# Kernel tuning notes

Measured on AMD Instinct MI355X. Metric: run time of the kernel, lower is better.

The kernel has to match this reference:

```python
import jax, jax.numpy as jnp
import numpy as np

B, N, D, H, NDIMS, NS = 4, 1024, 512, 8, 3, 1
HD = D // H


def setup_inputs() -> dict:
    key = jax.random.key(0)
    ks = jax.random.split(key, 10)
    x = jax.random.normal(ks[0], (B, N, D), dtype=jnp.float32)
    coords = jax.random.normal(ks[1], (B, N, NDIMS), dtype=jnp.float32)
    # pad last 64 key positions in half the batch
    key_padding_mask = jnp.zeros((B, N), dtype=bool).at[: B // 2, -64:].set(True)
    s = 1.0 / np.sqrt(D)
    Wqkv = jax.random.normal(ks[2], (3 * D, D), dtype=jnp.float32) * s  # torch Linear weight [out,in]
    Wout = jax.random.normal(ks[3], (D, D), dtype=jnp.float32) * s
    bout = jnp.zeros((D,), dtype=jnp.float32)
    fin = NDIMS + 1  # num_dims>1 -> dist channel appended
    W1 = jax.random.normal(ks[4], (H * 4, fin), dtype=jnp.float32) / np.sqrt(fin)
    b1 = jnp.zeros((H * 4,), dtype=jnp.float32)
    W2 = jax.random.normal(ks[5], (H, H * 4), dtype=jnp.float32) / np.sqrt(H * 4)
    b2 = jnp.zeros((H,), dtype=jnp.float32)
    bias_alpha = jax.random.normal(ks[6], (1,), dtype=jnp.float32)
    return dict(x=x, coords=coords, key_padding_mask=key_padding_mask,
                bias_alpha=bias_alpha, W1=W1, b1=b1, W2=W2, b2=b2,
                Wqkv=Wqkv, Wout=Wout, bout=bout)


def reference(x, coords, key_padding_mask, bias_alpha, W1, b1, W2, b2, Wqkv, Wout, bout):
    scale = HD ** (-0.5)
    qkv = x @ Wqkv.T  # [B,N,3D]
    q, k, v = jnp.split(qkv, 3, axis=-1)
    q = q.reshape(B, N, H, HD).transpose(0, 2, 1, 3)  # [B,H,N,HD]
    k = k.reshape(B, N, H, HD).transpose(0, 2, 1, 3)
    v = v.reshape(B, N, H, HD).transpose(0, 2, 1, 3)

    dpos = coords[:, :, None, :] - coords[:, None, :, :]  # [B,N,N,ndims]
    dist = jnp.linalg.norm(dpos, axis=-1, keepdims=True)
    dpos = jnp.concatenate([dpos, dist], axis=-1)  # [B,N,N,ndims+1]
    h = jax.nn.gelu(dpos @ W1.T + b1, approximate=False)
    bias = (h @ W2.T + b2).transpose(0, 3, 1, 2)  # [B,H,N,N]
    # zero bias rows/cols for special tokens
    valid = jnp.arange(N) >= NS
    bias = bias * (valid[:, None] & valid[None, :])[None, None]

    dots = jnp.einsum('bhid,bhjd->bhij', q, k) * scale
    logits = dots + bias_alpha[0] * bias
    logits = jnp.where(key_padding_mask[:, None, None, :], -jnp.inf, logits)
    attn = jax.nn.softmax(logits, axis=-1)
    out = jnp.einsum('bhij,bhjd->bhid', attn, v)
    out = out.transpose(0, 2, 1, 3).reshape(B, N, D)
    return out @ Wout.T + bout, attn
```

## Files before the change

### kernel.cpp

```cpp
#include <hip/hip_runtime.h>
#include <hip/hip_fp16.h>
#include <stdint.h>
#include <math.h>

#define B_  4
#define N_  1024
#define D_  512
#define H_  8
#define HD_ 64

typedef short s16x8 __attribute__((ext_vector_type(8)));
typedef float f32x4 __attribute__((ext_vector_type(4)));

__device__ __forceinline__ unsigned short f2bf(float f) {
    unsigned u = __float_as_uint(f);
    u += 0x7fffu + ((u >> 16) & 1u);
    return (unsigned short)(u >> 16);
}
__device__ __forceinline__ float bf2f(unsigned short h) {
    return __uint_as_float(((unsigned)h) << 16);
}

__device__ __forceinline__ float fast_gelu(float x) {
    float ax = fabsf(x) * 0.7071067811865476f;
    float t  = __builtin_amdgcn_rcpf(fmaf(0.3275911f, ax, 1.0f));
    float e  = __expf(-ax * ax);
    float poly = t * fmaf(t, fmaf(t, fmaf(t, fmaf(t, 1.061405429f, -1.453152027f),
                                          1.421413741f), -0.284496736f), 0.254829592f);
    float erfv = 1.0f - poly * e;
    float s = copysignf(erfv, x);
    return 0.5f * x * (1.0f + s);
}

__global__ void k_split(const float* __restrict__ s, unsigned short* __restrict__ h,
                        unsigned short* __restrict__ l, int n) {
    int i = blockIdx.x * 256 + threadIdx.x;
    if (i < n) {
        float x = s[i];
        unsigned short hb = f2bf(x);
        h[i] = hb;
        l[i] = f2bf(x - bf2f(hb));
    }
}

__global__ void k_mask_detect(const unsigned char* __restrict__ m, int* __restrict__ flag) {
    __shared__ int s;
    if (threadIdx.x == 0) s = 0;
    __syncthreads();
    int found = 0;
    for (int i = threadIdx.x; i < B_ * N_; i += 256)
        if ((i & 3) && m[i]) found = 1;
    if (found) atomicOr(&s, 1);
    __syncthreads();
    if (threadIdx.x == 0) flag[0] = s;
}

__global__ __launch_bounds__(256) void k_gemm3(
    const unsigned short* __restrict__ Ah, const unsigned short* __restrict__ Al,
    const unsigned short* __restrict__ Bwh, const unsigned short* __restrict__ Bwl,
    float* __restrict__ C, const float* __restrict__ bias, int M, int Nn, int K)
{
    constexpr int BM = 64, BN = 128, BK = 64;
    __shared__ unsigned short At[BM * BK];
    __shared__ unsigned short Bt[BN * BK];
    const int tid = threadIdx.x, lane = tid & 63, wid = tid >> 6;
    const int m0 = blockIdx.x * BM, n0 = blockIdx.y * BN;
    const int wm = wid >> 1, wn = wid & 1;
    f32x4 acc[2][4] = {};
    const unsigned short* Aps[3] = {Ah, Ah, Al};
    const unsigned short* Bps[3] = {Bwh, Bwl, Bwh};

    for (int combo = 0; combo < 3; ++combo) {
        const unsigned short* __restrict__ Ap = Aps[combo];
        const unsigned short* __restrict__ Bp = Bps[combo];
        for (int k0 = 0; k0 < K; k0 += BK) {
            s16x8 sa[2], sb[4];
            #pragma unroll
            for (int r = 0; r < 2; ++r) {
                int s = r * 256 + tid, row = s >> 3, c8 = s & 7;
                sa[r] = *(const s16x8*)(Ap + (size_t)(m0 + row) * K + k0 + c8 * 8);
            }
            #pragma unroll
            for (int r = 0; r < 4; ++r) {
                int s = r * 256 + tid, row = s >> 3, c8 = s & 7;
                sb[r] = *(const s16x8*)(Bp + (size_t)(n0 + row) * K + k0 + c8 * 8);
            }
            __syncthreads();
            #pragma unroll
            for (int r = 0; r < 2; ++r) { int s = r * 256 + tid; *(s16x8*)(At + s * 8) = sa[r]; }
            #pragma unroll
            for (int r = 0; r < 4; ++r) { int s = r * 256 + tid; *(s16x8*)(Bt + s * 8) = sb[r]; }
            __syncthreads();
            #pragma unroll
            for (int kk = 0; kk < BK; kk += 32) {
                s16x8 a[2], bb[4];
                #pragma unroll
                for (int fm = 0; fm < 2; ++fm)
                    a[fm] = *(const s16x8*)(At + (wm * 32 + fm * 16 + (lane & 15)) * BK + kk + (lane >> 4) * 8);
                #pragma unroll
                for (int fn = 0; fn < 4; ++fn)
                    bb[fn] = *(const s16x8*)(Bt + (wn * 64 + fn * 16 + (lane & 15)) * BK + kk + (lane >> 4) * 8);
                #pragma unroll
                for (int fm = 0; fm < 2; ++fm)
                    #pragma unroll
                    for (int fn = 0; fn < 4; ++fn)
                        acc[fm][fn] = __builtin_amdgcn_mfma_f32_16x16x32_bf16(a[fm], bb[fn], acc[fm][fn], 0, 0, 0);
            }
        }
    }
    #pragma unroll
    for (int fm = 0; fm < 2; ++fm)
        #pragma unroll
        for (int fn = 0; fn < 4; ++fn)
            #pragma unroll
            for (int r = 0; r < 4; ++r) {
                int row  = m0 + wm * 32 + fm * 16 + (lane >> 4) * 4 + r;
                int coln = n0 + wn * 64 + fn * 16 + (lane & 15);
                float v = acc[fm][fn][r];
                if (bias) v += bias[coln];
                C[(size_t)row * Nn + coln] = v;
            }
}

__global__ void k_rearrange(const float* __restrict__ qkv, unsigned short* __restrict__ qp,
                            unsigned short* __restrict__ kp) {
    int t = blockIdx.x * 256 + threadIdx.x;
    int d = t & 63, n = (t >> 6) & 1023, h = (t >> 16) & 7, b = t >> 19;
    const float* src = qkv + ((size_t)(b * N_ + n)) * (3 * D_) + h * HD_ + d;
    float q = src[0], k = src[D_];
    unsigned short qh = f2bf(q), ql = f2bf(q - bf2f(qh));
    unsigned short kh = f2bf(k), kl = f2bf(k - bf2f(kh));
    size_t base = ((size_t)(b * H_ + h) * N_ + n) * 128;
    qp[base + d] = qh; qp[base + 64 + d] = ql;
    kp[base + d] = kh; kp[base + 64 + d] = kl;
}

__global__ void k_vtrans(const float* __restrict__ qkv, unsigned short* __restrict__ vT) {
    __shared__ unsigned short T[64][65];
    int n0 = blockIdx.x * 64, h = blockIdx.y, b = blockIdx.z;
    int tid = threadIdx.x;
    #pragma unroll
    for (int rep = 0; rep < 16; ++rep) {
        int idx = rep * 256 + tid;
        int nl = idx >> 6, d = idx & 63;
        T[nl][d] = f2bf(qkv[((size_t)(b * N_ + n0 + nl)) * (3 * D_) + 2 * D_ + h * HD_ + d]);
    }
    __syncthreads();
    #pragma unroll
    for (int rep = 0; rep < 16; ++rep) {
        int idx = rep * 256 + tid;
        int dl = idx >> 6, nl = idx & 63;
        vT[((size_t)(b * H_ + h) * HD_ + dl) * N_ + n0 + nl] = T[nl][dl];
    }
}

__global__ __launch_bounds__(256) void k_bias(
    const float* __restrict__ coords, const float* __restrict__ alpha,
    const float* __restrict__ W1, const float* __restrict__ b1,
    const float* __restrict__ W2, const float* __restrict__ b2,
    unsigned short* __restrict__ biasH)
{
    __shared__ float sW1[128], sb1[32], sW2[256], sb2[8];
    int tid = threadIdx.x;
    if (tid < 128) sW1[tid] = W1[tid];
    if (tid < 32)  sb1[tid] = b1[tid];
    sW2[tid] = W2[tid];
    if (tid < 8)   sb2[tid] = b2[tid];
    __syncthreads();

    size_t t = (size_t)blockIdx.x * 256 + tid;
    int j = (int)(t & 1023), i = (int)((t >> 10) & 1023), b = (int)(t >> 20);
    const float* ci = coords + ((size_t)b * N_ + i) * 3;
    const float* cj = coords + ((size_t)b * N_ + j) * 3;
    float dx = ci[0] - cj[0], dy = ci[1] - cj[1], dz = ci[2] - cj[2];
    float dist = sqrtf(dx * dx + dy * dy + dz * dz);

    float acc[8];
    #pragma unroll
    for (int hh = 0; hh < 8; ++hh) acc[hh] = sb2[hh];

    #pragma unroll 1
    for (int g = 0; g < 4; ++g) {
        float gg[8];
        #pragma unroll
        for (int cc = 0; cc < 8; ++cc) {
            int c = g * 8 + cc;
            float p = fmaf(sW1[c * 4], dx,
                      fmaf(sW1[c * 4 + 1], dy,
                      fmaf(sW1[c * 4 + 2], dz,
                      fmaf(sW1[c * 4 + 3], dist, sb1[c]))));
            gg[cc] = fast_gelu(p);
        }
        #pragma unroll
        for (int hh = 0; hh < 8; ++hh)
            #pragma unroll
            for (int cc = 0; cc < 8; ++cc)
                acc[hh] = fmaf(sW2[hh * 32 + g * 8 + cc], gg[cc], acc[hh]);
    }

    float vfac = (i >= 1 && j >= 1) ? alpha[0] : 0.f;
    #pragma unroll
    for (int hh = 0; hh < 8; ++hh) {
        __half hv = __float2half(vfac * acc[hh]);
        biasH[(((size_t)(b * H_ + hh)) * N_ + i) * N_ + j] = *(unsigned short*)&hv;
    }
}

__global__ __launch_bounds__(256, 3) void k_attn(
    const unsigned short* __restrict__ qp, const unsigned short* __restrict__ kp,
    const unsigned short* __restrict__ vT,
    const unsigned short* __restrict__ biasH,
    float* __restrict__ attnout,
    const unsigned char* __restrict__ mraw, const int* __restrict__ flag,
    unsigned short* __restrict__ avh, unsigned short* __restrict__ avl)
{
    __shared__ s16x8 pool16[2048];
    __shared__ unsigned char smask[N_];
    __shared__ float redm[16][4];
    __shared__ float reds[16][4];
    const int tid = threadIdx.x, lane = tid & 63, wid = tid >> 6;

    int flat = blockIdx.x + 64 * (blockIdx.y + 8 * blockIdx.z);
    int swz  = (flat & 7) * 256 + (flat >> 3);
    const int i0 = (swz & 63) * 16;
    const int h  = (swz >> 6) & 7;
    const int b  = swz >> 9;
    const size_t bh = (size_t)(b * H_ + h);
    const int g = lane >> 4;
    const int cl = lane & 15;

    if (flag[0] != 0) {
        for (int i2 = tid; i2 < N_; i2 += 256) smask[i2] = mraw[b * N_ + i2];
    } else {
        const int* mi = (const int*)mraw;
        for (int i2 = tid; i2 < N_; i2 += 256) smask[i2] = (unsigned char)(mi[b * N_ + i2] != 0);
    }

    const unsigned short* qrow = qp + (bh * N_ + i0 + cl) * 128 + g * 8;
    s16x8 aqh0 = *(const s16x8*)(qrow);
    s16x8 aqh1 = *(const s16x8*)(qrow + 32);
    s16x8 aql0 = *(const s16x8*)(qrow + 64);
    s16x8 aql1 = *(const s16x8*)(qrow + 96);

    int soff[4];
    #pragma unroll
    for (int p = 0; p < 4; ++p) {
        int o = p * 4096 + tid * 16;
        int row = o >> 8, offl = o & 255;
        soff[p] = row * 128 + ((offl ^ ((row & 7) << 4)) >> 1);
    }
    const unsigned short* kbase = kp + bh * (size_t)N_ * 128;

    const int lr = wid * 16 + cl;
    int rdoff[4];
    #pragma unroll
    for (int f = 0; f < 4; ++f)
        rdoff[f] = lr * 256 + ((g * 16 + f * 64) ^ ((lr & 7) << 4));

    char* poolb = (char*)pool16;

    {
        s16x8 st[4];
        #pragma unroll
        for (int p = 0; p < 4; ++p) st[p] = *(const s16x8*)(kbase + soff[p]);
        #pragma unroll
        for (int p = 0; p < 4; ++p) *(s16x8*)(poolb + p * 4096 + tid * 16) = st[p];
    }
    __syncthreads();

    f32x4 acc[16];
    #pragma unroll
    for (int c = 0; c < 16; ++c) {
        s16x8 st[4];
        if (c < 15) {
            const unsigned short* cb = kbase + (size_t)(c + 1) * 8192;
            #pragma unroll
            for (int p = 0; p < 4; ++p) st[p] = *(const s16x8*)(cb + soff[p]);
        }
        char* kb = poolb + (c & 1) * 16384;
        s16x8 k0 = *(const s16x8*)(kb + rdoff[0]);
        s16x8 k1 = *(const s16x8*)(kb + rdoff[1]);
        s16x8 k2 = *(const s16x8*)(kb + rdoff[2]);
        s16x8 k3 = *(const s16x8*)(kb + rdoff[3]);
        f32x4 a = {0.f, 0.f, 0.f, 0.f};
        a = __builtin_amdgcn_mfma_f32_16x16x32_bf16(aqh0, k0, a, 0, 0, 0);
        a = __builtin_amdgcn_mfma_f32_16x16x32_bf16(aqh1, k1, a, 0, 0, 0);
        a = __builtin_amdgcn_mfma_f32_16x16x32_bf16(aqh0, k2, a, 0, 0, 0);
        a = __builtin_amdgcn_mfma_f32_16x16x32_bf16(aqh1, k3, a, 0, 0, 0);
        a = __builtin_amdgcn_mfma_f32_16x16x32_bf16(aql0, k0, a, 0, 0, 0);
        a = __builtin_amdgcn_mfma_f32_16x16x32_bf16(aql1, k1, a, 0, 0, 0);
        acc[c] = a;
        if (c < 15) {
            char* wb = poolb + ((c + 1) & 1) * 16384;
            #pragma unroll
            for (int p = 0; p < 4; ++p) *(s16x8*)(wb + p * 4096 + tid * 16) = st[p];
        }
        __syncthreads();
    }

    {
        unsigned short* bl = (unsigned short*)poolb;
        const unsigned short* bsrc = biasH + (bh * N_ + i0) * N_;
        #pragma unroll
        for (int p2 = 0; p2 < 8; ++p2) {
            int idx = p2 * 256 + tid;
            *(s16x8*)(bl + idx * 8) = *(const s16x8*)(bsrc + (size_t)idx * 8);
        }
    }
    __syncthreads();

    const float scale = 0.125f;
    const unsigned short* bl = (const unsigned short*)poolb;
    #pragma unroll
    for (int j = 0; j < 16; ++j) {
        const int col = (j * 4 + wid) * 16 + cl;
        const bool mj = (smask[col] != 0);
        #pragma unroll
        for (int r = 0; r < 4; ++r) {
            unsigned short u = bl[(g * 4 + r) * 1024 + col];
            float bv = __half2float(*(const __half*)&u);
            acc[j][r] = mj ? -1e30f : fmaf(acc[j][r], scale, bv);
        }
    }

    float m[4];
    #pragma unroll
    for (int r = 0; r < 4; ++r) {
        float mm = acc[0][r];
        #pragma unroll
        for (int j = 1; j < 16; ++j) mm = fmaxf(mm, acc[j][r]);
        m[r] = mm;
    }
    #pragma unroll
    for (int msk = 1; msk < 16; msk <<= 1)
        #pragma unroll
        for (int r = 0; r < 4; ++r) m[r] = fmaxf(m[r], __shfl_xor(m[r], msk));
    if (cl == 0)
        #pragma unroll
        for (int r = 0; r < 4; ++r) redm[g * 4 + r][wid] = m[r];
    __syncthreads();
    #pragma unroll
    for (int r = 0; r < 4; ++r) {
        int row = g * 4 + r;
        m[r] = fmaxf(fmaxf(redm[row][0], redm[row][1]), fmaxf(redm[row][2], redm[row][3]));
    }

    float s[4] = {0.f, 0.f, 0.f, 0.f};
    #pragma unroll
    for (int j = 0; j < 16; ++j)
        #pragma unroll
        for (int r = 0; r < 4; ++r) {
            float e = __expf(acc[j][r] - m[r]);
            acc[j][r] = e;
            s[r] += e;
        }
    #pragma unroll
    for (int msk = 1; msk < 16; msk <<= 1)
        #pragma unroll
        for (int r = 0; r < 4; ++r) s[r] += __shfl_xor(s[r], msk);
    if (cl == 0)
        #pragma unroll
        for (int r = 0; r < 4; ++r) reds[g * 4 + r][wid] = s[r];
    __syncthreads();
    float sinv[4];
    #pragma unroll
    for (int r = 0; r < 4; ++r) {
        int row = g * 4 + r;
        sinv[r] = 1.0f / (reds[row][0] + reds[row][1] + reds[row][2] + reds[row][3]);
    }

    float* gattn = attnout + (bh * N_ + i0) * N_;
    char* Pb = poolb;
    #pragma unroll
    for (int j = 0; j < 16; ++j) {
        const int col = (j * 4 + wid) * 16 + cl;
        #pragma unroll
        for (int r = 0; r < 4; ++r) {
            const int row = g * 4 + r;
            float e = acc[j][r];
            gattn[(size_t)row * N_ + col] = e * sinv[r];
            int byte = row * 2048 + ((col * 2) ^ ((row & 7) << 4));
            *(unsigned short*)(Pb + byte) = f2bf(e);
        }
    }
    __syncthreads();

    {
        const int d0 = wid * 16;
        f32x4 acc2 = {0.f, 0.f, 0.f, 0.f};
        const unsigned short* vrow = vT + (bh * HD_ + d0 + cl) * N_ + g * 8;
        const int rowA = cl;
        const int swzb = (rowA & 7) << 4;
        for (int kk = 0; kk < N_; kk += 32) {
            s16x8 bfrag = *(const s16x8*)(vrow + kk);
            int byte = rowA * 2048 + (((kk + g * 8) * 2) ^ swzb);
            s16x8 af = *(const s16x8*)(Pb + byte);
            acc2 = __builtin_amdgcn_mfma_f32_16x16x32_bf16(af, bfrag, acc2, 0, 0, 0);
        }
        #pragma unroll
        for (int r = 0; r < 4; ++r) {
            const int row = g * 4 + r;
            const int dd = d0 + cl;
            float v = acc2[r] * sinv[r];
            unsigned short hv = f2bf(v);
            size_t o = ((size_t)(b * N_) + i0 + row) * D_ + h * HD_ + dd;
            avh[o] = hv;
            avl[o] = f2bf(v - bf2f(hv));
        }
    }
}

extern "C" void kernel_launch(void* const* d_in, const int* in_sizes, int n_in,
                              void* d_out, int out_size, void* d_ws, size_t ws_size,
                              hipStream_t stream) {
    (void)in_sizes; (void)n_in; (void)out_size; (void)ws_size;
    const float* x      = (const float*)d_in[0];
    const float* coords = (const float*)d_in[1];
    const unsigned char* kpm = (const unsigned char*)d_in[2];
    const float* alpha  = (const float*)d_in[3];
    const float* W1     = (const float*)d_in[4];
    const float* b1     = (const float*)d_in[5];
    const float* W2     = (const float*)d_in[6];
    const float* b2     = (const float*)d_in[7];
    const float* Wqkv   = (const float*)d_in[8];
    const float* Wout   = (const float*)d_in[9];
    const float* bout   = (const float*)d_in[10];

    float* out  = (float*)d_out;
    float* attn = out + (size_t)B_ * N_ * D_;

    char* w = (char*)d_ws;
    auto alloc = [&](size_t bytes) { char* p = w; w += (bytes + 255) & ~(size_t)255; return p; };
    const size_t SZ_X  = (size_t)B_ * N_ * D_;
    const size_t SZ_WQ = (size_t)3 * D_ * D_;
    const size_t SZ_WO = (size_t)D_ * D_;

    unsigned short* wo_hi = (unsigned short*)alloc(SZ_WO * 2);
    unsigned short* wo_lo = (unsigned short*)alloc(SZ_WO * 2);
    unsigned short* qp = (unsigned short*)alloc((size_t)B_ * H_ * N_ * 128 * 2);
    unsigned short* kp = (unsigned short*)alloc((size_t)B_ * H_ * N_ * 128 * 2);
    unsigned short* vT = (unsigned short*)alloc((size_t)B_ * H_ * HD_ * N_ * 2);
    unsigned short* av_hi = (unsigned short*)alloc(SZ_X * 2);
    unsigned short* av_lo = (unsigned short*)alloc(SZ_X * 2);
    int* flag = (int*)alloc(256);

    char* uni = (char*)alloc(0);
    unsigned short* x_hi = (unsigned short*)uni;
    unsigned short* x_lo = x_hi + SZ_X;
    unsigned short* wq_hi = x_lo + SZ_X;
    unsigned short* wq_lo = wq_hi + SZ_WQ;
    float* qkv = (float*)(wq_lo + SZ_WQ);
    unsigned short* biasH = (unsigned short*)uni;

    k_split<<<(int)((SZ_X + 255) / 256), 256, 0, stream>>>(x, x_hi, x_lo, (int)SZ_X);
    k_split<<<(int)((SZ_WQ + 255) / 256), 256, 0, stream>>>(Wqkv, wq_hi, wq_lo, (int)SZ_WQ);
    k_split<<<(int)((SZ_WO + 255) / 256), 256, 0, stream>>>(Wout, wo_hi, wo_lo, (int)SZ_WO);
    k_mask_detect<<<1, 256, 0, stream>>>(kpm, flag);
    k_gemm3<<<dim3(64, 12), 256, 0, stream>>>(x_hi, x_lo, wq_hi, wq_lo, qkv, nullptr,
                                              B_ * N_, 3 * D_, D_);
    k_rearrange<<<(B_ * H_ * N_ * HD_) / 256, 256, 0, stream>>>(qkv, qp, kp);
    k_vtrans<<<dim3(16, H_, B_), 256, 0, stream>>>(qkv, vT);
    k_bias<<<(B_ * N_ * N_) / 256, 256, 0, stream>>>(coords, alpha, W1, b1, W2, b2, biasH);
    k_attn<<<dim3(64, H_, B_), 256, 0, stream>>>(qp, kp, vT, biasH, attn, kpm, flag, av_hi, av_lo);
    k_gemm3<<<dim3(64, 4), 256, 0, stream>>>(av_hi, av_lo, wo_hi, wo_lo, out, bout,
                                             B_ * N_, D_, D_);
}
```

Baseline: 279.1 us.

## Factor bias MLP first layer per node and replace GELU with LUT interpolation

Splits the first linear layer of the positional-bias MLP into a per-node projection (computed once by a new kernel and stored in fp16) and a per-pair distance term, so each pair needs only a subtraction plus one FMA per channel. The erf-based GELU is replaced by a 256-entry shared-memory table with linear interpolation over a clamped range and identity-like extrapolation above it. The second layer uses packed fp16 dot products. This cuts ALU work in the O(B·N²) bias kernel in exchange for reduced precision (fp16 projections, LUT approximation, clamping below -4) and per-block table setup.

```diff
diff --git a/kernel.cpp b/kernel.cpp
--- a/kernel.cpp
+++ b/kernel.cpp
@@ -11,6 +11,8 @@
 
 typedef short s16x8 __attribute__((ext_vector_type(8)));
 typedef float f32x4 __attribute__((ext_vector_type(4)));
+typedef float f32x2 __attribute__((ext_vector_type(2)));
+typedef __fp16 f16x2 __attribute__((ext_vector_type(2)));
 
 __device__ __forceinline__ unsigned short f2bf(float f) {
     unsigned u = __float_as_uint(f);
@@ -154,22 +156,63 @@
     }
 }
 
+__global__ void k_nodeproj(const float* __restrict__ coords, const float* __restrict__ W1,
+                           unsigned short* __restrict__ Pt) {
+    int t = blockIdx.x * 256 + threadIdx.x;
+    int bn = t & 4095, c = t >> 12;
+    const float* cc = coords + (size_t)bn * 3;
+    float v = 32.f * (W1[c * 4] * cc[0] + W1[c * 4 + 1] * cc[1] + W1[c * 4 + 2] * cc[2]);
+    __half hv = __float2half(v);
+    Pt[t] = *(unsigned short*)&hv;
+}
+
 __global__ __launch_bounds__(256) void k_bias(
     const float* __restrict__ coords, const float* __restrict__ alpha,
     const float* __restrict__ W1, const float* __restrict__ b1,
     const float* __restrict__ W2, const float* __restrict__ b2,
+    const unsigned short* __restrict__ Pt,
     unsigned short* __restrict__ biasH)
 {
-    __shared__ float sW1[128], sb1[32], sW2[256], sb2[8];
-    int tid = threadIdx.x;
-    if (tid < 128) sW1[tid] = W1[tid];
-    if (tid < 32)  sb1[tid] = b1[tid];
-    sW2[tid] = W2[tid];
-    if (tid < 8)   sb2[tid] = b2[tid];
-    __syncthreads();
-
-    size_t t = (size_t)blockIdx.x * 256 + tid;
-    int j = (int)(t & 1023), i = (int)((t >> 10) & 1023), b = (int)(t >> 20);
+    __shared__ unsigned short sPj[32 * 256];
+    __shared__ float lut[512];
+    __shared__ float SPi[32], swd32[32], sb2f[8];
+    __shared__ unsigned short sW2h[8 * 32];
+    const int tid = threadIdx.x;
+    const int bid = blockIdx.x;
+    const int j0 = (bid & 3) * 256;
+    const int i  = (bid >> 2) & 1023;
+    const int b  = bid >> 12;
+
+    {
+        float xk = (tid - 128) * 0.03125f;
+        float g0 = fast_gelu(xk);
+        float g1 = fast_gelu(xk + 0.03125f);
+        lut[tid * 2]     = g0;
+        lut[tid * 2 + 1] = g1 - g0;
+    }
+    if (tid < 32) {
+        const float* ci = coords + ((size_t)b * N_ + i) * 3;
+        float w0 = W1[tid * 4], w1 = W1[tid * 4 + 1], w2 = W1[tid * 4 + 2], w3 = W1[tid * 4 + 3];
+        SPi[tid]   = 32.f * (w0 * ci[0] + w1 * ci[1] + w2 * ci[2] + b1[tid]) + 128.f;
+        swd32[tid] = 32.f * w3;
+    }
+    if (tid < 8) sb2f[tid] = b2[tid];
+    {
+        __half hv = __float2half(W2[tid]);
+        sW2h[tid] = *(unsigned short*)&hv;
+    }
+    {
+        #pragma unroll
+        for (int p = 0; p < 4; ++p) {
+            int idx = p * 256 + tid;
+            int row = idx >> 5, off = (idx & 31) * 8;
+            *(s16x8*)(sPj + row * 256 + off) =
+                *(const s16x8*)(Pt + (size_t)row * (B_ * N_) + b * N_ + j0 + off);
+        }
+    }
+    __syncthreads();
+
+    const int j = j0 + tid;
     const float* ci = coords + ((size_t)b * N_ + i) * 3;
     const float* cj = coords + ((size_t)b * N_ + j) * 3;
     float dx = ci[0] - cj[0], dy = ci[1] - cj[1], dz = ci[2] - cj[2];
@@ -177,32 +220,44 @@
 
     float acc[8];
     #pragma unroll
-    for (int hh = 0; hh < 8; ++hh) acc[hh] = sb2[hh];
+    for (int h = 0; h < 8; ++h) acc[h] = 0.f;
 
     #pragma unroll 1
     for (int g = 0; g < 4; ++g) {
-        float gg[8];
+        f16x2 gh[4];
+        float gprev = 0.f;
         #pragma unroll
         for (int cc = 0; cc < 8; ++cc) {
             int c = g * 8 + cc;
-            float p = fmaf(sW1[c * 4], dx,
-                      fmaf(sW1[c * 4 + 1], dy,
-                      fmaf(sW1[c * 4 + 2], dz,
-                      fmaf(sW1[c * 4 + 3], dist, sb1[c]))));
-            gg[cc] = fast_gelu(p);
-        }
-        #pragma unroll
-        for (int hh = 0; hh < 8; ++hh)
-            #pragma unroll
-            for (int cc = 0; cc < 8; ++cc)
-                acc[hh] = fmaf(sW2[hh * 32 + g * 8 + cc], gg[cc], acc[hh]);
+            unsigned short u = sPj[c * 256 + tid];
+            float pj = __half2float(*(const __half*)&u);
+            float t  = fmaf(swd32[c], dist, SPi[c] - pj);
+            float tc = fminf(fmaxf(t, 0.f), 255.f);
+            float fi = floorf(tc);
+            int   ii = (int)fi;
+            float fr = tc - fi;
+            f32x2 vs = *(const f32x2*)(lut + ii * 2);
+            float gg = fmaf(fr, vs[1], vs[0]);
+            float xb = fmaf(t, 0.03125f, -4.f);
+            gg = (t > 254.f) ? xb : gg;
+            if (cc & 1) gh[cc >> 1] = __builtin_amdgcn_cvt_pkrtz(gprev, gg);
+            else        gprev = gg;
+        }
+        #pragma unroll
+        for (int h = 0; h < 8; ++h) {
+            const f16x2* wp = (const f16x2*)(sW2h + h * 32 + g * 8);
+            acc[h] = __builtin_amdgcn_fdot2(gh[0], wp[0], acc[h], false);
+            acc[h] = __builtin_amdgcn_fdot2(gh[1], wp[1], acc[h], false);
+            acc[h] = __builtin_amdgcn_fdot2(gh[2], wp[2], acc[h], false);
+            acc[h] = __builtin_amdgcn_fdot2(gh[3], wp[3], acc[h], false);
+        }
     }
 
     float vfac = (i >= 1 && j >= 1) ? alpha[0] : 0.f;
     #pragma unroll
-    for (int hh = 0; hh < 8; ++hh) {
-        __half hv = __float2half(vfac * acc[hh]);
-        biasH[(((size_t)(b * H_ + hh)) * N_ + i) * N_ + j] = *(unsigned short*)&hv;
+    for (int h = 0; h < 8; ++h) {
+        __half hv = __float2half(vfac * (acc[h] + sb2f[h]));
+        biasH[(((size_t)(b * H_ + h)) * N_ + i) * N_ + j] = *(unsigned short*)&hv;
     }
 }
 
@@ -442,6 +497,7 @@
     unsigned short* vT = (unsigned short*)alloc((size_t)B_ * H_ * HD_ * N_ * 2);
     unsigned short* av_hi = (unsigned short*)alloc(SZ_X * 2);
     unsigned short* av_lo = (unsigned short*)alloc(SZ_X * 2);
+    unsigned short* Pt = (unsigned short*)alloc((size_t)32 * B_ * N_ * 2);
     int* flag = (int*)alloc(256);
 
     char* uni = (char*)alloc(0);
@@ -456,11 +512,12 @@
     k_split<<<(int)((SZ_WQ + 255) / 256), 256, 0, stream>>>(Wqkv, wq_hi, wq_lo, (int)SZ_WQ);
     k_split<<<(int)((SZ_WO + 255) / 256), 256, 0, stream>>>(Wout, wo_hi, wo_lo, (int)SZ_WO);
     k_mask_detect<<<1, 256, 0, stream>>>(kpm, flag);
+    k_nodeproj<<<(32 * B_ * N_) / 256, 256, 0, stream>>>(coords, W1, Pt);
     k_gemm3<<<dim3(64, 12), 256, 0, stream>>>(x_hi, x_lo, wq_hi, wq_lo, qkv, nullptr,
                                               B_ * N_, 3 * D_, D_);
     k_rearrange<<<(B_ * H_ * N_ * HD_) / 256, 256, 0, stream>>>(qkv, qp, kp);
     k_vtrans<<<dim3(16, H_, B_), 256, 0, stream>>>(qkv, vT);
-    k_bias<<<(B_ * N_ * N_) / 256, 256, 0, stream>>>(coords, alpha, W1, b1, W2, b2, biasH);
+    k_bias<<<(B_ * N_ * N_) / 256, 256, 0, stream>>>(coords, alpha, W1, b1, W2, b2, Pt, biasH);
     k_attn<<<dim3(64, H_, B_), 256, 0, stream>>>(qp, kp, vT, biasH, attn, kpm, flag, av_hi, av_lo);
     k_gemm3<<<dim3(64, 4), 256, 0, stream>>>(av_hi, av_lo, wo_hi, wo_lo, out, bout,
                                              B_ * N_, D_, D_);
```

New measurement: 242.5 us. -13.1%, faster.
